# Optimization experiments

Hardware: AMD Instinct MI355X
Metric: run time of the kernel (lower is better)

## Reference

```python
import jax, jax.numpy as jnp
import numpy as np
from jax import lax

N_SPINS = 32   # num_spins
HILDIM = 2     # hilbert space dim
HID = 512      # hidden_size
NLAYERS = 3    # num_layers
NSAMP = 2048   # numsamples (acts as the RNN time axis, per torch's unbatched semantics)


def setup_inputs() -> dict:
    key = jax.random.key(0)
    ks = jax.random.split(key, 11)
    k = 1.0 / np.sqrt(HID)  # torch.nn.RNN default init bound
    u = lambda kk, shape: jax.random.uniform(kk, shape, jnp.float32, -k, k)
    return {
        "samples": jax.random.randint(ks[0], (NSAMP, N_SPINS), 0, HILDIM),
        "Wih0": u(ks[1], (N_SPINS, HID, HILDIM)),        # layer-0 input weights per spin
        "Whh0": u(ks[2], (N_SPINS, HID, HID)),
        "bih0": u(ks[3], (N_SPINS, HID)),
        "bhh0": u(ks[4], (N_SPINS, HID)),
        "Wih": u(ks[5], (N_SPINS, NLAYERS - 1, HID, HID)),  # layers 1..L-1 per spin
        "Whh": u(ks[6], (N_SPINS, NLAYERS - 1, HID, HID)),
        "bih": u(ks[7], (N_SPINS, NLAYERS - 1, HID)),
        "bhh": u(ks[8], (N_SPINS, NLAYERS - 1, HID)),
        "Wd": u(ks[9], (N_SPINS, 2, HID)),                  # dense head per spin
        "bd": u(ks[10], (N_SPINS, 2)),
    }


def _rnn_scan(x_seq, h0, Wi, Wh, bi, bh):
    # Faithful torch.nn.RNN (tanh) over the sample axis (torch treats the 2D
    # [numsamples, feat] input as an unbatched sequence of length numsamples).
    def step(h, x):
        h = jnp.tanh(x @ Wi.T + bi + h @ Wh.T + bh)
        return h, h
    hT, ys = lax.scan(step, h0, x_seq)
    return ys, hT  # ys: [S, H], hT: [H]


def reference(samples, Wih0, Whh0, bih0, bhh0, Wih, Whh, bih, bhh, Wd, bd):
    # Implements RNN.probability(samples)
    S, N = samples.shape
    H = Whh0.shape[-1]
    hd = Wih0.shape[-1]
    L = Wih.shape[1] + 1
    onehot = jax.nn.one_hot(samples, hd, dtype=jnp.float32)          # [S, N, hd]
    # inputs fed to spin i: zeros for i=0, one_hot(samples[:, i-1]) after
    xs = jnp.concatenate([jnp.zeros((1, S, hd), jnp.float32),
                          jnp.transpose(onehot, (1, 0, 2))[:-1]], axis=0)  # [N, S, hd]

    def spin_step(state, per):
        # state: [L, H] hidden carried across spins (as in the torch code)
        x, Wi0, Wh0, bi0, bh0, WiL, WhL, biL, bhL, Wdi, bdi = per
        new_state = []
        y, hT = _rnn_scan(x, state[0], Wi0, Wh0, bi0, bh0)
        new_state.append(hT)
        for l in range(WiL.shape[0]):  # small static loop over layers 1..L-1
            y, hT = _rnn_scan(y, state[l + 1], WiL[l], WhL[l], biL[l], bhL[l])
            new_state.append(hT)
        p = jax.nn.softmax(y @ Wdi.T + bdi, axis=-1)  # [S, 2]
        return jnp.stack(new_state), p

    state0 = jnp.zeros((L, H), jnp.float32)
    _, probs = lax.scan(
        spin_step, state0,
        (xs, Wih0, Whh0, bih0, bhh0, Wih, Whh, bih, bhh, Wd, bd))
    probs = jnp.transpose(probs, (1, 0, 2))                          # [S, N, 2]
    return jnp.prod(jnp.sum(probs * onehot, axis=2), axis=1)         # [S]
```

## Files before the change

kernel.cpp:

```cpp
#include <hip/hip_runtime.h>
#include <stdint.h>

typedef unsigned long long u64;

#define SPS   2048
#define NSPIN 32
#define H     512
#define NSTEP (SPS*NSPIN)
#define TPB   512
#define NL    3
#define LB    32
#define RPB   16
#define HEAD  (NL*LB)
#define NB    (NL*LB + 1)

__device__ __forceinline__ u64 ld_agent(const u64* p){
  return __hip_atomic_load(p, __ATOMIC_RELAXED, __HIP_MEMORY_SCOPE_AGENT);
}
__device__ __forceinline__ void st_agent(u64* p, u64 v){
  __hip_atomic_store(p, v, __ATOMIC_RELAXED, __HIP_MEMORY_SCOPE_AGENT);
}
__device__ __forceinline__ unsigned ldu_agent(const unsigned* p){
  return __hip_atomic_load(p, __ATOMIC_RELAXED, __HIP_MEMORY_SCOPE_AGENT);
}
__device__ __forceinline__ void stu_agent(unsigned* p, unsigned v){
  __hip_atomic_store(p, v, __ATOMIC_RELAXED, __HIP_MEMORY_SCOPE_AGENT);
}

__device__ __forceinline__ float poll_pkt(const u64* p, unsigned tag){
  u64 v = ld_agent(p);
  int n = 0;
  while ((unsigned)(v >> 32) != tag){
    if (++n > 8) __builtin_amdgcn_s_sleep(1);
    v = ld_agent(p);
    if (n > (1<<22)) break;
  }
  return __uint_as_float((unsigned)(v & 0xffffffffu));
}

__global__ void init_prog(unsigned* prog){
  for (int j = threadIdx.x; j < NB*16; j += 512) prog[j] = 0;
}

__global__ __launch_bounds__(TPB, 2)
void rnn_pipeline(const int* __restrict__ samples,
                  const float* __restrict__ Wih0, const float* __restrict__ Whh0,
                  const float* __restrict__ bih0, const float* __restrict__ bhh0,
                  const float* __restrict__ Wih,  const float* __restrict__ Whh,
                  const float* __restrict__ bih,  const float* __restrict__ bhh,
                  const float* __restrict__ Wd,   const float* __restrict__ bd,
                  float* __restrict__ out,
                  u64* __restrict__ ring, unsigned* __restrict__ prog,
                  int depth)
{
  const int bid = blockIdx.x;
  const int tid = threadIdx.x;
  const int dmask = depth - 1;

  __shared__ __align__(16) float lds_h[2][H];
  __shared__ __align__(16) float lds_y[2][H];
  __shared__ float lds_res[RPB];
  __shared__ int   lds_bits[SPS];
  __shared__ float lds_acc[SPS];
  __shared__ float lds_red[2][2][8];

  if (bid == HEAD){
    for (int tt = tid; tt < SPS; tt += TPB) lds_acc[tt] = 1.0f;
    __syncthreads();
    u64* ring2 = ring + (size_t)2*depth*H;
    const int w = tid >> 6, lane = tid & 63;
    float wd0=0.f, wd1=0.f, b0=0.f, b1=0.f;
    for (int u = 0; u < NSTEP; ++u){
      const int i = u >> 11, t = u & (SPS-1), par = u & 1;
      if ((u & (SPS-1)) == 0){
        __syncthreads();
        for (int tt = tid; tt < SPS; tt += TPB)
          lds_bits[tt] = samples[tt*NSPIN + i];
        wd0 = Wd[((size_t)i*2+0)*H + tid];
        wd1 = Wd[((size_t)i*2+1)*H + tid];
        b0 = bd[i*2+0]; b1 = bd[i*2+1];
      }
      const float y = poll_pkt(&ring2[(size_t)(u & dmask)*H + tid], (unsigned)(u+1));
      if (tid == 511 && (u & 31) == 31) stu_agent(&prog[HEAD*16], (unsigned)(u+1));
      float p0 = wd0*y, p1 = wd1*y;
      #pragma unroll
      for (int o = 32; o > 0; o >>= 1){
        p0 += __shfl_down(p0, o);
        p1 += __shfl_down(p1, o);
      }
      if (lane == 0){ lds_red[par][0][w] = p0; lds_red[par][1][w] = p1; }
      __syncthreads();
      if (tid == 0){
        float z0 = b0, z1 = b1;
        #pragma unroll
        for (int q = 0; q < 8; ++q){ z0 += lds_red[par][0][q]; z1 += lds_red[par][1][q]; }
        const float m  = fmaxf(z0, z1);
        const float e0 = expf(z0 - m), e1 = expf(z1 - m);
        lds_acc[t] *= (lds_bits[t] ? e1 : e0) / (e0 + e1);
      }
    }
    if (tid == 511) stu_agent(&prog[HEAD*16], (unsigned)NSTEP);
    __syncthreads();
    for (int tt = tid; tt < SPS; tt += TPB) out[tt] = lds_acc[tt];
    return;
  }

  const int layer = bid >> 5;
  const int g     = bid & 31;
  const int c     = tid & 31;
  const int sub   = tid >> 5;
  const int row   = g*RPB + sub;
  const bool leader = (c == 0);
  const bool has_wi = (layer > 0);
  u64* ringL  = ring + (size_t)layer*depth*H;
  u64* ringIn = ring + (size_t)(layer > 0 ? layer-1 : 0)*depth*H;
  const int rot = (c >> 2) & 3;

  float wh[16], wi[16];
  float bsum = 0.f, w0c = 0.f, w1c = 0.f;

  for (int u = 0; u < NSTEP; ++u){
    const int i = u >> 11, t = u & (SPS-1), par = u & 1;

    if ((u & (SPS-1)) == 0){
      __syncthreads();
      if (layer == 0 && i > 0){
        for (int tt = tid; tt < SPS; tt += TPB)
          lds_bits[tt] = samples[tt*NSPIN + (i-1)];
      }
      const float* wrow = (layer == 0)
        ? Whh0 + ((size_t)i*H + row)*H
        : Whh  + (((size_t)i*(NL-1) + (layer-1))*H + row)*H;
      #pragma unroll
      for (int jj = 0; jj < 4; ++jj){
        const int s = (jj + rot) & 3;
        const float4 v = *(const float4*)(wrow + c*16 + s*4);
        wh[4*jj+0]=v.x; wh[4*jj+1]=v.y; wh[4*jj+2]=v.z; wh[4*jj+3]=v.w;
      }
      if (has_wi){
        const float* irow = Wih + (((size_t)i*(NL-1) + (layer-1))*H + row)*H;
        #pragma unroll
        for (int jj = 0; jj < 4; ++jj){
          const int s = (jj + rot) & 3;
          const float4 v = *(const float4*)(irow + c*16 + s*4);
          wi[4*jj+0]=v.x; wi[4*jj+1]=v.y; wi[4*jj+2]=v.z; wi[4*jj+3]=v.w;
        }
      }
      if (leader){
        if (layer == 0){
          bsum = bih0[i*H + row] + bhh0[i*H + row];
          w0c  = Wih0[((size_t)i*H + row)*2 + 0];
          w1c  = Wih0[((size_t)i*H + row)*2 + 1];
        } else {
          bsum = bih[((size_t)i*(NL-1)+(layer-1))*H + row]
               + bhh[((size_t)i*(NL-1)+(layer-1))*H + row];
        }
      }
    }

    {
      const u64* ph = &ringL[(size_t)((u-1) & dmask)*H + tid];
      const u64* pq = &ringIn[(size_t)(u & dmask)*H + tid];
      const bool needh = (u > 0);
      const unsigned tagh = (unsigned)u, tagy = (unsigned)(u+1);
      u64 vh = needh  ? ld_agent(ph) : 0;
      u64 vy = has_wi ? ld_agent(pq) : 0;
      bool okh = !needh, oky = !has_wi;
      float rh = 0.f, ry = 0.f;
      int n = 0;
      for (;;){
        if (!okh && (unsigned)(vh >> 32) == tagh){ okh = true; rh = __uint_as_float((unsigned)vh); }
        if (!oky && (unsigned)(vy >> 32) == tagy){ oky = true; ry = __uint_as_float((unsigned)vy); }
        if (okh && oky) break;
        if (++n > 8) __builtin_amdgcn_s_sleep(1);
        if (!okh) vh = ld_agent(ph);
        if (!oky) vy = ld_agent(pq);
        if (n > (1<<22)) break;
      }
      lds_h[par][tid] = rh;
      if (has_wi) lds_y[par][tid] = ry;
    }

    if (tid == 510 && (u & 31) == 31) stu_agent(&prog[bid*16], (unsigned)(u+1));
    if (tid == 509 && (u & 63) == 0 && (u + 64) > depth){
      const unsigned need = (unsigned)(u + 64 - depth);
      const int cfirst = (layer < 2) ? (layer+1)*LB : HEAD;
      const int ccount = (layer < 2) ? LB : 1;
      int guard = 0;
      for (;;){
        unsigned mn = 0xffffffffu;
        for (int q = 0; q < ccount; ++q){
          const unsigned pv = ldu_agent(&prog[(cfirst+q)*16]);
          mn = pv < mn ? pv : mn;
        }
        if (mn >= need) break;
        __builtin_amdgcn_s_sleep(8);
        if (++guard > (1<<20)) break;
      }
    }

    __syncthreads();

    const float* hbase = &lds_h[par][c*16];
    float a0=0.f, a1=0.f, a2=0.f, a3=0.f;
    #pragma unroll
    for (int jj = 0; jj < 4; ++jj){
      const int s = (jj + rot) & 3;
      const float4 hv = *(const float4*)(hbase + s*4);
      a0 = fmaf(wh[4*jj+0], hv.x, a0); a1 = fmaf(wh[4*jj+1], hv.y, a1);
      a2 = fmaf(wh[4*jj+2], hv.z, a2); a3 = fmaf(wh[4*jj+3], hv.w, a3);
    }
    if (has_wi){
      const float* ybase = &lds_y[par][c*16];
      #pragma unroll
      for (int jj = 0; jj < 4; ++jj){
        const int s = (jj + rot) & 3;
        const float4 yv = *(const float4*)(ybase + s*4);
        a0 = fmaf(wi[4*jj+0], yv.x, a0); a1 = fmaf(wi[4*jj+1], yv.y, a1);
        a2 = fmaf(wi[4*jj+2], yv.z, a2); a3 = fmaf(wi[4*jj+3], yv.w, a3);
      }
    }
    float p = (a0 + a1) + (a2 + a3);
    p += __shfl_down(p, 16);
    p += __shfl_down(p, 8);
    p += __shfl_down(p, 4);
    p += __shfl_down(p, 2);
    p += __shfl_down(p, 1);

    if (leader){
      float s = p + bsum;
      if (layer == 0 && i > 0) s += lds_bits[t] ? w1c : w0c;
      lds_res[sub] = tanhf(s);
    }
    __syncthreads();

    if (tid < RPB){
      st_agent(&ringL[(size_t)(u & dmask)*H + g*RPB + tid],
               ((u64)(unsigned)(u+1) << 32) | (u64)__float_as_uint(lds_res[tid]));
    }
  }
  if (tid == 510) stu_agent(&prog[bid*16], (unsigned)NSTEP);
}

extern "C" void kernel_launch(void* const* d_in, const int* in_sizes, int n_in,
                              void* d_out, int out_size, void* d_ws, size_t ws_size,
                              hipStream_t stream)
{
  const int*   samples = (const int*)  d_in[0];
  const float* Wih0    = (const float*)d_in[1];
  const float* Whh0    = (const float*)d_in[2];
  const float* bih0    = (const float*)d_in[3];
  const float* bhh0    = (const float*)d_in[4];
  const float* Wih     = (const float*)d_in[5];
  const float* Whh     = (const float*)d_in[6];
  const float* bih     = (const float*)d_in[7];
  const float* bhh     = (const float*)d_in[8];
  const float* Wd      = (const float*)d_in[9];
  const float* bd      = (const float*)d_in[10];

  int depth = 256;
  while (depth > 2 && (size_t)3*depth*H*sizeof(u64) + 8192 > ws_size) depth >>= 1;

  u64*      ring = (u64*)d_ws;
  unsigned* prog = (unsigned*)((char*)d_ws + (size_t)3*depth*H*sizeof(u64));

  init_prog<<<1, 512, 0, stream>>>(prog);
  rnn_pipeline<<<NB, TPB, 0, stream>>>(samples, Wih0, Whh0, bih0, bhh0,
                                       Wih, Whh, bih, bhh, Wd, bd,
                                       (float*)d_out, ring, prog, depth);
}
```

Baseline: 111.1 ms.

## Use 8 blocks per layer and precompute next-step input projection off the critical path

Each layer now runs on 8 blocks of 64 rows instead of 32 blocks of 16 rows, with 8 lanes per row holding 64 weights each. This shrinks the cross-block reduction and the number of blocks taking part in ring polling. The input-projection dot product for step u+1 is computed right after publishing step u's output, so only the recurrent Whh product sits on the serial dependency chain. The cost is more registers per thread, fewer CUs doing the work, and the y ring being polled one step ahead.

```diff
diff --git a/kernel.cpp b/kernel.cpp
--- a/kernel.cpp
+++ b/kernel.cpp
@@ -9,10 +9,21 @@
 #define NSTEP (SPS*NSPIN)
 #define TPB   512
 #define NL    3
-#define LB    32
-#define RPB   16
+#define LB    8
+#define RPB   64
 #define HEAD  (NL*LB)
 #define NB    (NL*LB + 1)
+
+#define REP16(X) X(0) X(1) X(2) X(3) X(4) X(5) X(6) X(7) X(8) X(9) X(10) X(11) X(12) X(13) X(14) X(15)
+#define DECL_W(j)  float4 wh##j = {0,0,0,0}, wi##j = {0,0,0,0};
+#define LOAD_WH(j) wh##j = *(const float4*)(whb + ((j + c) & 15)*4);
+#define LOAD_WI(j) wi##j = *(const float4*)(wib + ((j + c) & 15)*4);
+#define FMA_WH(j)  { const float4 hv = *(const float4*)(hb2 + ((j + c) & 15)*4); \
+                     a0 = fmaf(wh##j.x, hv.x, a0); a1 = fmaf(wh##j.y, hv.y, a1); \
+                     a2 = fmaf(wh##j.z, hv.z, a2); a3 = fmaf(wh##j.w, hv.w, a3); }
+#define FMA_WI(j)  { const float4 yv = *(const float4*)(yb + ((j + c) & 15)*4);  \
+                     b0 = fmaf(wi##j.x, yv.x, b0); b1 = fmaf(wi##j.y, yv.y, b1); \
+                     b2 = fmaf(wi##j.z, yv.z, b2); b3 = fmaf(wi##j.w, yv.w, b3); }
 
 __device__ __forceinline__ u64 ld_agent(const u64* p){
   return __hip_atomic_load(p, __ATOMIC_RELAXED, __HIP_MEMORY_SCOPE_AGENT);
@@ -105,19 +116,22 @@
     return;
   }
 
-  const int layer = bid >> 5;
-  const int g     = bid & 31;
-  const int c     = tid & 31;
-  const int sub   = tid >> 5;
-  const int row   = g*RPB + sub;
+  const int layer = bid >> 3, g = bid & 7;
+  const int c   = tid & 7;
+  const int r   = tid >> 3;
+  const int row = g*RPB + r;
   const bool leader = (c == 0);
   const bool has_wi = (layer > 0);
   u64* ringL  = ring + (size_t)layer*depth*H;
   u64* ringIn = ring + (size_t)(layer > 0 ? layer-1 : 0)*depth*H;
-  const int rot = (c >> 2) & 3;
-
-  float wh[16], wi[16];
-  float bsum = 0.f, w0c = 0.f, w1c = 0.f;
+
+  REP16(DECL_W)
+  float bsum = 0.f, w0c = 0.f, w1c = 0.f, py = 0.f;
+
+  if (has_wi){
+    lds_y[0][tid] = poll_pkt(&ringIn[(size_t)0*H + tid], 1u);
+    __syncthreads();
+  }
 
   for (int u = 0; u < NSTEP; ++u){
     const int i = u >> 11, t = u & (SPS-1), par = u & 1;
@@ -128,23 +142,17 @@
         for (int tt = tid; tt < SPS; tt += TPB)
           lds_bits[tt] = samples[tt*NSPIN + (i-1)];
       }
-      const float* wrow = (layer == 0)
+      const float* whb = ((layer == 0)
         ? Whh0 + ((size_t)i*H + row)*H
-        : Whh  + (((size_t)i*(NL-1) + (layer-1))*H + row)*H;
-      #pragma unroll
-      for (int jj = 0; jj < 4; ++jj){
-        const int s = (jj + rot) & 3;
-        const float4 v = *(const float4*)(wrow + c*16 + s*4);
-        wh[4*jj+0]=v.x; wh[4*jj+1]=v.y; wh[4*jj+2]=v.z; wh[4*jj+3]=v.w;
-      }
+        : Whh  + (((size_t)i*(NL-1) + (layer-1))*H + row)*H) + c*64;
+      REP16(LOAD_WH)
       if (has_wi){
-        const float* irow = Wih + (((size_t)i*(NL-1) + (layer-1))*H + row)*H;
-        #pragma unroll
-        for (int jj = 0; jj < 4; ++jj){
-          const int s = (jj + rot) & 3;
-          const float4 v = *(const float4*)(irow + c*16 + s*4);
-          wi[4*jj+0]=v.x; wi[4*jj+1]=v.y; wi[4*jj+2]=v.z; wi[4*jj+3]=v.w;
-        }
+        const float* wib = Wih + (((size_t)i*(NL-1) + (layer-1))*H + row)*H + c*64;
+        REP16(LOAD_WI)
+        const float* yb = &lds_y[u & 1][c*64];
+        float b0=0.f, b1=0.f, b2=0.f, b3=0.f;
+        REP16(FMA_WI)
+        py = (b0 + b1) + (b2 + b3);
       }
       if (leader){
         if (layer == 0){
@@ -160,12 +168,13 @@
 
     {
       const u64* ph = &ringL[(size_t)((u-1) & dmask)*H + tid];
-      const u64* pq = &ringIn[(size_t)(u & dmask)*H + tid];
+      const u64* pq = &ringIn[(size_t)((u+1) & dmask)*H + tid];
       const bool needh = (u > 0);
-      const unsigned tagh = (unsigned)u, tagy = (unsigned)(u+1);
-      u64 vh = needh  ? ld_agent(ph) : 0;
-      u64 vy = has_wi ? ld_agent(pq) : 0;
-      bool okh = !needh, oky = !has_wi;
+      const bool needy = has_wi && (u+1) < NSTEP;
+      const unsigned tagh = (unsigned)u, tagy = (unsigned)(u+2);
+      u64 vh = needh ? ld_agent(ph) : 0;
+      u64 vy = needy ? ld_agent(pq) : 0;
+      bool okh = !needh, oky = !needy;
       float rh = 0.f, ry = 0.f;
       int n = 0;
       for (;;){
@@ -178,7 +187,7 @@
         if (n > (1<<22)) break;
       }
       lds_h[par][tid] = rh;
-      if (has_wi) lds_y[par][tid] = ry;
+      if (needy) lds_y[(u+1) & 1][tid] = ry;
     }
 
     if (tid == 510 && (u & 31) == 31) stu_agent(&prog[bid*16], (unsigned)(u+1));
@@ -201,42 +210,30 @@
 
     __syncthreads();
 
-    const float* hbase = &lds_h[par][c*16];
-    float a0=0.f, a1=0.f, a2=0.f, a3=0.f;
-    #pragma unroll
-    for (int jj = 0; jj < 4; ++jj){
-      const int s = (jj + rot) & 3;
-      const float4 hv = *(const float4*)(hbase + s*4);
-      a0 = fmaf(wh[4*jj+0], hv.x, a0); a1 = fmaf(wh[4*jj+1], hv.y, a1);
-      a2 = fmaf(wh[4*jj+2], hv.z, a2); a3 = fmaf(wh[4*jj+3], hv.w, a3);
-    }
-    if (has_wi){
-      const float* ybase = &lds_y[par][c*16];
-      #pragma unroll
-      for (int jj = 0; jj < 4; ++jj){
-        const int s = (jj + rot) & 3;
-        const float4 yv = *(const float4*)(ybase + s*4);
-        a0 = fmaf(wi[4*jj+0], yv.x, a0); a1 = fmaf(wi[4*jj+1], yv.y, a1);
-        a2 = fmaf(wi[4*jj+2], yv.z, a2); a3 = fmaf(wi[4*jj+3], yv.w, a3);
-      }
-    }
+    const float* hb2 = &lds_h[par][c*64];
+    float a0 = py, a1 = 0.f, a2 = 0.f, a3 = 0.f;
+    REP16(FMA_WH)
     float p = (a0 + a1) + (a2 + a3);
-    p += __shfl_down(p, 16);
-    p += __shfl_down(p, 8);
     p += __shfl_down(p, 4);
     p += __shfl_down(p, 2);
     p += __shfl_down(p, 1);
-
     if (leader){
       float s = p + bsum;
       if (layer == 0 && i > 0) s += lds_bits[t] ? w1c : w0c;
-      lds_res[sub] = tanhf(s);
+      lds_res[r] = tanhf(s);
     }
     __syncthreads();
 
     if (tid < RPB){
       st_agent(&ringL[(size_t)(u & dmask)*H + g*RPB + tid],
                ((u64)(unsigned)(u+1) << 32) | (u64)__float_as_uint(lds_res[tid]));
+    }
+
+    if (has_wi && (u+1) < NSTEP && ((u+1) & (SPS-1)) != 0){
+      const float* yb = &lds_y[(u+1) & 1][c*64];
+      float b0=0.f, b1=0.f, b2=0.f, b3=0.f;
+      REP16(FMA_WI)
+      py = (b0 + b1) + (b2 + b3);
     }
   }
   if (tid == 510) stu_agent(&prog[bid*16], (unsigned)NSTEP);
```

After: 170.0 ms. 1.53x slower.

## Pin each RNN layer to one XCD and poll recurrent state via L2-local fast ring

Applied to the files above, without the earlier changes.

Launches 256 blocks and keeps only those whose blockIdx maps to XCDs 0-3. Each layer's 32 blocks therefore sit on one XCD (round-robin dispatch is assumed), and the head block sits on XCD 3. The intra-layer hidden-state exchange is written to a second ring with sc0 stores and polled with sc0 loads, so it can be served from the shared per-XCD L2 instead of going through device-scope coherence. A slow agent-scope copy is still written and checked every 8 polls as a fallback. Backpressure sleep and timeout constants also change, and a vmcnt wait is added after every step's stores. The design relies on how hardware places blocks and on cache-coherence semantics, and it doubles the workspace, which may halve the ring depth.

```diff
diff --git a/kernel.cpp b/kernel.cpp
--- a/kernel.cpp
+++ b/kernel.cpp
@@ -11,8 +11,9 @@
 #define NL    3
 #define LB    32
 #define RPB   16
-#define HEAD  (NL*LB)
-#define NB    (NL*LB + 1)
+#define NROLE 97
+#define HEADROLE 96
+#define GRID  256
 
 __device__ __forceinline__ u64 ld_agent(const u64* p){
   return __hip_atomic_load(p, __ATOMIC_RELAXED, __HIP_MEMORY_SCOPE_AGENT);
@@ -25,6 +26,18 @@
 }
 __device__ __forceinline__ void stu_agent(unsigned* p, unsigned v){
   __hip_atomic_store(p, v, __ATOMIC_RELAXED, __HIP_MEMORY_SCOPE_AGENT);
+}
+
+__device__ __forceinline__ u64 ld_sc0(const u64* p){
+  u64 v;
+  asm volatile("global_load_dwordx2 %0, %1, off sc0\n\t"
+               "s_waitcnt vmcnt(0)"
+               : "=v"(v) : "v"(p) : "memory");
+  return v;
+}
+__device__ __forceinline__ void st_sc0(u64* p, u64 v){
+  asm volatile("global_store_dwordx2 %0, %1, off sc0"
+               :: "v"(p), "v"(v) : "memory");
 }
 
 __device__ __forceinline__ float poll_pkt(const u64* p, unsigned tag){
@@ -39,7 +52,7 @@
 }
 
 __global__ void init_prog(unsigned* prog){
-  for (int j = threadIdx.x; j < NB*16; j += 512) prog[j] = 0;
+  for (int j = threadIdx.x; j < NROLE*16; j += 512) prog[j] = 0;
 }
 
 __global__ __launch_bounds__(TPB, 2)
@@ -50,12 +63,19 @@
                   const float* __restrict__ bih,  const float* __restrict__ bhh,
                   const float* __restrict__ Wd,   const float* __restrict__ bd,
                   float* __restrict__ out,
-                  u64* __restrict__ ring, unsigned* __restrict__ prog,
-                  int depth)
+                  u64* __restrict__ ring, u64* __restrict__ fastb,
+                  unsigned* __restrict__ prog, int depth)
 {
   const int bid = blockIdx.x;
   const int tid = threadIdx.x;
   const int dmask = depth - 1;
+
+  const int xcd = bid & 7, idx = bid >> 3;
+  if (xcd > 3 || (xcd == 3 && idx > 0)) return;
+  const bool ishead = (xcd == 3);
+  const int layer = ishead ? 0 : xcd;
+  const int g     = idx;
+  const int role  = ishead ? HEADROLE : layer*LB + g;
 
   __shared__ __align__(16) float lds_h[2][H];
   __shared__ __align__(16) float lds_y[2][H];
@@ -64,7 +84,7 @@
   __shared__ float lds_acc[SPS];
   __shared__ float lds_red[2][2][8];
 
-  if (bid == HEAD){
+  if (ishead){
     for (int tt = tid; tt < SPS; tt += TPB) lds_acc[tt] = 1.0f;
     __syncthreads();
     u64* ring2 = ring + (size_t)2*depth*H;
@@ -81,7 +101,7 @@
         b0 = bd[i*2+0]; b1 = bd[i*2+1];
       }
       const float y = poll_pkt(&ring2[(size_t)(u & dmask)*H + tid], (unsigned)(u+1));
-      if (tid == 511 && (u & 31) == 31) stu_agent(&prog[HEAD*16], (unsigned)(u+1));
+      if (tid == 511 && (u & 31) == 31) stu_agent(&prog[HEADROLE*16], (unsigned)(u+1));
       float p0 = wd0*y, p1 = wd1*y;
       #pragma unroll
       for (int o = 32; o > 0; o >>= 1){
@@ -99,21 +119,20 @@
         lds_acc[t] *= (lds_bits[t] ? e1 : e0) / (e0 + e1);
       }
     }
-    if (tid == 511) stu_agent(&prog[HEAD*16], (unsigned)NSTEP);
+    if (tid == 511) stu_agent(&prog[HEADROLE*16], (unsigned)NSTEP);
     __syncthreads();
     for (int tt = tid; tt < SPS; tt += TPB) out[tt] = lds_acc[tt];
     return;
   }
 
-  const int layer = bid >> 5;
-  const int g     = bid & 31;
   const int c     = tid & 31;
   const int sub   = tid >> 5;
   const int row   = g*RPB + sub;
   const bool leader = (c == 0);
   const bool has_wi = (layer > 0);
-  u64* ringL  = ring + (size_t)layer*depth*H;
-  u64* ringIn = ring + (size_t)(layer > 0 ? layer-1 : 0)*depth*H;
+  u64* ringL  = ring  + (size_t)layer*depth*H;
+  u64* fastL  = fastb + (size_t)layer*depth*H;
+  u64* ringIn = ring  + (size_t)(layer > 0 ? layer-1 : 0)*depth*H;
   const int rot = (c >> 2) & 3;
 
   float wh[16], wi[16];
@@ -159,32 +178,40 @@
     }
 
     {
-      const u64* ph = &ringL[(size_t)((u-1) & dmask)*H + tid];
-      const u64* pq = &ringIn[(size_t)(u & dmask)*H + tid];
+      const size_t sh = (size_t)((u-1) & dmask)*H + tid;
+      const u64* phF = fastL + sh;
+      const u64* phS = ringL + sh;
+      const u64* pq  = &ringIn[(size_t)(u & dmask)*H + tid];
       const bool needh = (u > 0);
       const unsigned tagh = (unsigned)u, tagy = (unsigned)(u+1);
-      u64 vh = needh  ? ld_agent(ph) : 0;
-      u64 vy = has_wi ? ld_agent(pq) : 0;
       bool okh = !needh, oky = !has_wi;
       float rh = 0.f, ry = 0.f;
       int n = 0;
-      for (;;){
-        if (!okh && (unsigned)(vh >> 32) == tagh){ okh = true; rh = __uint_as_float((unsigned)vh); }
-        if (!oky && (unsigned)(vy >> 32) == tagy){ oky = true; ry = __uint_as_float((unsigned)vy); }
+      while (!(okh && oky)){
+        if (!okh){
+          u64 v = ld_sc0(phF);
+          if ((unsigned)(v >> 32) == tagh){ okh = true; rh = __uint_as_float((unsigned)v); }
+          else if ((n & 7) == 7){
+            v = ld_agent(phS);
+            if ((unsigned)(v >> 32) == tagh){ okh = true; rh = __uint_as_float((unsigned)v); }
+          }
+        }
+        if (!oky){
+          u64 v = ld_agent(pq);
+          if ((unsigned)(v >> 32) == tagy){ oky = true; ry = __uint_as_float((unsigned)v); }
+        }
         if (okh && oky) break;
-        if (++n > 8) __builtin_amdgcn_s_sleep(1);
-        if (!okh) vh = ld_agent(ph);
-        if (!oky) vy = ld_agent(pq);
-        if (n > (1<<22)) break;
+        if (n > 2) __builtin_amdgcn_s_sleep(1);
+        if (++n > (1<<20)) break;
       }
       lds_h[par][tid] = rh;
       if (has_wi) lds_y[par][tid] = ry;
     }
 
-    if (tid == 510 && (u & 31) == 31) stu_agent(&prog[bid*16], (unsigned)(u+1));
+    if (tid == 510 && (u & 31) == 31) stu_agent(&prog[role*16], (unsigned)(u+1));
     if (tid == 509 && (u & 63) == 0 && (u + 64) > depth){
       const unsigned need = (unsigned)(u + 64 - depth);
-      const int cfirst = (layer < 2) ? (layer+1)*LB : HEAD;
+      const int cfirst = (layer < 2) ? (layer+1)*LB : HEADROLE;
       const int ccount = (layer < 2) ? LB : 1;
       int guard = 0;
       for (;;){
@@ -194,8 +221,8 @@
           mn = pv < mn ? pv : mn;
         }
         if (mn >= need) break;
-        __builtin_amdgcn_s_sleep(8);
-        if (++guard > (1<<20)) break;
+        __builtin_amdgcn_s_sleep(16);
+        if (++guard > (1<<18)) break;
       }
     }
 
@@ -235,11 +262,15 @@
     __syncthreads();
 
     if (tid < RPB){
-      st_agent(&ringL[(size_t)(u & dmask)*H + g*RPB + tid],
-               ((u64)(unsigned)(u+1) << 32) | (u64)__float_as_uint(lds_res[tid]));
-    }
+      const u64 pkt = ((u64)(unsigned)(u+1) << 32)
+                    | (u64)__float_as_uint(lds_res[tid]);
+      const size_t so = (size_t)(u & dmask)*H + g*RPB + tid;
+      st_sc0(fastL + so, pkt);
+      st_agent(ringL + so, pkt);
+    }
+    asm volatile("s_waitcnt vmcnt(0)" ::: "memory");
   }
-  if (tid == 510) stu_agent(&prog[bid*16], (unsigned)NSTEP);
+  if (tid == 510) stu_agent(&prog[role*16], (unsigned)NSTEP);
 }
 
 extern "C" void kernel_launch(void* const* d_in, const int* in_sizes, int n_in,
@@ -259,13 +290,14 @@
   const float* bd      = (const float*)d_in[10];
 
   int depth = 256;
-  while (depth > 2 && (size_t)3*depth*H*sizeof(u64) + 8192 > ws_size) depth >>= 1;
-
-  u64*      ring = (u64*)d_ws;
-  unsigned* prog = (unsigned*)((char*)d_ws + (size_t)3*depth*H*sizeof(u64));
+  while (depth > 2 && (size_t)6*depth*H*sizeof(u64) + 8192 > ws_size) depth >>= 1;
+
+  u64*      ring  = (u64*)d_ws;
+  u64*      fastb = ring + (size_t)3*depth*H;
+  unsigned* prog  = (unsigned*)((char*)d_ws + (size_t)6*depth*H*sizeof(u64));
 
   init_prog<<<1, 512, 0, stream>>>(prog);
-  rnn_pipeline<<<NB, TPB, 0, stream>>>(samples, Wih0, Whh0, bih0, bhh0,
-                                       Wih, Whh, bih, bhh, Wd, bd,
-                                       (float*)d_out, ring, prog, depth);
-}
+  rnn_pipeline<<<GRID, TPB, 0, stream>>>(samples, Wih0, Whh0, bih0, bhh0,
+                                         Wih, Whh, bih, bhh, Wd, bd,
+                                         (float*)d_out, ring, fastb, prog, depth);
+}
```

Result: slower. 161.5 ms (+45.4%).

## Assign pipeline roles by XCC id so each layer stays on one chiplet

Applied to the files above, without the earlier changes.

The kernel now launches a larger grid. Each block reads its hardware XCC id and claims a role from a per-XCC atomic pool, so all 32 blocks of a layer share one XCD and the head sits on another. Surplus blocks exit right away. The aim is to keep the heavy intra-layer h-vector traffic within one XCD's L2 and to cut cross-die latency in the polling handoffs. The risk is that this relies on how the hardware places blocks on XCDs and on enough blocks landing on each XCD to be co-resident; if not, roles stay unfilled and the pipeline deadlocks.

```diff
diff --git a/kernel.cpp b/kernel.cpp
--- a/kernel.cpp
+++ b/kernel.cpp
@@ -11,8 +11,9 @@
 #define NL    3
 #define LB    32
 #define RPB   16
-#define HEAD  (NL*LB)
-#define NB    (NL*LB + 1)
+#define NROLE 97
+#define HEADROLE 96
+#define GRID  512
 
 __device__ __forceinline__ u64 ld_agent(const u64* p){
   return __hip_atomic_load(p, __ATOMIC_RELAXED, __HIP_MEMORY_SCOPE_AGENT);
@@ -39,7 +40,7 @@
 }
 
 __global__ void init_prog(unsigned* prog){
-  for (int j = threadIdx.x; j < NB*16; j += 512) prog[j] = 0;
+  for (int j = threadIdx.x; j < NROLE*16 + 16; j += 512) prog[j] = 0;
 }
 
 __global__ __launch_bounds__(TPB, 2)
@@ -51,9 +52,8 @@
                   const float* __restrict__ Wd,   const float* __restrict__ bd,
                   float* __restrict__ out,
                   u64* __restrict__ ring, unsigned* __restrict__ prog,
-                  int depth)
+                  int* __restrict__ pool, int depth)
 {
-  const int bid = blockIdx.x;
   const int tid = threadIdx.x;
   const int dmask = depth - 1;
 
@@ -63,8 +63,27 @@
   __shared__ int   lds_bits[SPS];
   __shared__ float lds_acc[SPS];
   __shared__ float lds_red[2][2][8];
-
-  if (bid == HEAD){
+  __shared__ int   role_s;
+
+  if (tid == 0){
+    int x;
+    asm volatile("s_getreg_b32 %0, hwreg(HW_REG_XCC_ID)" : "=s"(x));
+    x &= 7;
+    int r = -1;
+    if (x < NL){
+      const int slot = atomicAdd(&pool[x], 1);
+      if (slot < LB) r = x*LB + slot;
+    } else if (x == NL){
+      const int slot = atomicAdd(&pool[x], 1);
+      if (slot == 0) r = HEADROLE;
+    }
+    role_s = r;
+  }
+  __syncthreads();
+  const int role = role_s;
+  if (role < 0) return;
+
+  if (role == HEADROLE){
     for (int tt = tid; tt < SPS; tt += TPB) lds_acc[tt] = 1.0f;
     __syncthreads();
     u64* ring2 = ring + (size_t)2*depth*H;
@@ -81,7 +100,7 @@
         b0 = bd[i*2+0]; b1 = bd[i*2+1];
       }
       const float y = poll_pkt(&ring2[(size_t)(u & dmask)*H + tid], (unsigned)(u+1));
-      if (tid == 511 && (u & 31) == 31) stu_agent(&prog[HEAD*16], (unsigned)(u+1));
+      if (tid == 511 && (u & 31) == 31) stu_agent(&prog[HEADROLE*16], (unsigned)(u+1));
       float p0 = wd0*y, p1 = wd1*y;
       #pragma unroll
       for (int o = 32; o > 0; o >>= 1){
@@ -99,14 +118,14 @@
         lds_acc[t] *= (lds_bits[t] ? e1 : e0) / (e0 + e1);
       }
     }
-    if (tid == 511) stu_agent(&prog[HEAD*16], (unsigned)NSTEP);
+    if (tid == 511) stu_agent(&prog[HEADROLE*16], (unsigned)NSTEP);
     __syncthreads();
     for (int tt = tid; tt < SPS; tt += TPB) out[tt] = lds_acc[tt];
     return;
   }
 
-  const int layer = bid >> 5;
-  const int g     = bid & 31;
+  const int layer = role >> 5;
+  const int g     = role & 31;
   const int c     = tid & 31;
   const int sub   = tid >> 5;
   const int row   = g*RPB + sub;
@@ -181,10 +200,10 @@
       if (has_wi) lds_y[par][tid] = ry;
     }
 
-    if (tid == 510 && (u & 31) == 31) stu_agent(&prog[bid*16], (unsigned)(u+1));
+    if (tid == 510 && (u & 31) == 31) stu_agent(&prog[role*16], (unsigned)(u+1));
     if (tid == 509 && (u & 63) == 0 && (u + 64) > depth){
       const unsigned need = (unsigned)(u + 64 - depth);
-      const int cfirst = (layer < 2) ? (layer+1)*LB : HEAD;
+      const int cfirst = (layer < 2) ? (layer+1)*LB : HEADROLE;
       const int ccount = (layer < 2) ? LB : 1;
       int guard = 0;
       for (;;){
@@ -239,7 +258,7 @@
                ((u64)(unsigned)(u+1) << 32) | (u64)__float_as_uint(lds_res[tid]));
     }
   }
-  if (tid == 510) stu_agent(&prog[bid*16], (unsigned)NSTEP);
+  if (tid == 510) stu_agent(&prog[role*16], (unsigned)NSTEP);
 }
 
 extern "C" void kernel_launch(void* const* d_in, const int* in_sizes, int n_in,
@@ -259,13 +278,14 @@
   const float* bd      = (const float*)d_in[10];
 
   int depth = 256;
-  while (depth > 2 && (size_t)3*depth*H*sizeof(u64) + 8192 > ws_size) depth >>= 1;
+  while (depth > 2 && (size_t)3*depth*H*sizeof(u64) + 16384 > ws_size) depth >>= 1;
 
   u64*      ring = (u64*)d_ws;
   unsigned* prog = (unsigned*)((char*)d_ws + (size_t)3*depth*H*sizeof(u64));
+  int*      pool = (int*)(prog + NROLE*16);
 
   init_prog<<<1, 512, 0, stream>>>(prog);
-  rnn_pipeline<<<NB, TPB, 0, stream>>>(samples, Wih0, Whh0, bih0, bhh0,
-                                       Wih, Whh, bih, bhh, Wd, bd,
-                                       (float*)d_out, ring, prog, depth);
-}
+  rnn_pipeline<<<GRID, TPB, 0, stream>>>(samples, Wih0, Whh0, bih0, bhh0,
+                                         Wih, Whh, bih, bhh, Wd, bd,
+                                         (float*)d_out, ring, prog, pool, depth);
+}
```

Measured after the change: 127.5 ms. +14.8%, slower.
